# Optimization experiments

Measured on AMD Instinct MI355X. Metric: run time of the kernel, lower is better.

The kernel has to match this reference:

```python
import jax, jax.numpy as jnp
import numpy as np

LN_EPS = 1e-5

def setup_inputs() -> dict:
    key = jax.random.key(0)
    B, S, D = 4, 2048, 1024
    ks = jax.random.split(key, 8)
    sc = 1.0 / np.sqrt(D)
    inp = {
        'x': jax.random.normal(ks[0], (B, S, D), jnp.float32),
        'Wq': jax.random.normal(ks[1], (D, D), jnp.float32) * sc,
        'bq': jnp.zeros((D,), jnp.float32),
        'Wk': jax.random.normal(ks[2], (D, D), jnp.float32) * sc,
        'bk': jnp.zeros((D,), jnp.float32),
        'Wv': jax.random.normal(ks[3], (D, D), jnp.float32) * sc,
        'bv': jnp.zeros((D,), jnp.float32),
        'Wo': jax.random.normal(ks[4], (D, D), jnp.float32) * sc,
        'bo': jnp.zeros((D,), jnp.float32),
        'Wg_val': jax.random.normal(ks[5], (D, D), jnp.float32) * sc,
        'bg_val': jnp.zeros((D,), jnp.float32),
        'Wg_gate': jax.random.normal(ks[6], (D, D), jnp.float32) * sc,
        'bg_gate': jnp.zeros((D,), jnp.float32),
        'gamma': jnp.ones((D,), jnp.float32),
        'beta': jnp.zeros((D,), jnp.float32),
    }
    return inp


def reference(x, Wq, bq, Wk, bk, Wv, bv, Wo, bo, Wg_val, bg_val, Wg_gate, bg_gate, gamma, beta):
    # x: [B,S,D]
    q = jnp.einsum('bsd,de->bse', x, Wq) + bq
    k = jnp.einsum('bsd,de->bse', x, Wk) + bk
    v = jnp.einsum('bsd,de->bse', x, Wv) + bv
    scale = 1.0 / jnp.sqrt(jnp.asarray(q.shape[-1], q.dtype))
    qk = jnp.einsum('bqe,bke->bqk', q, k) * scale  # [B,S,S]
    a = jax.nn.softmax(qk, axis=-1)
    out = jnp.einsum('bqk,bke->bqe', a, v)
    out = jnp.einsum('bse,ed->bsd', out, Wo) + bo
    # GLU residual on q, then LayerNorm
    glu = (jnp.einsum('bse,ed->bsd', q, Wg_val) + bg_val) * jax.nn.sigmoid(jnp.einsum('bse,ed->bsd', q, Wg_gate) + bg_gate)
    out = out + glu
    mu = jnp.mean(out, axis=-1, keepdims=True)
    var = jnp.var(out, axis=-1, keepdims=True)
    out = (out - mu) * jax.lax.rsqrt(var + LN_EPS) * gamma + beta
    return out
```

## Files before the change

### kernel.cpp

```cpp
#include <hip/hip_runtime.h>
#include <hip/hip_bf16.h>
#include <cstdint>


typedef __bf16 bf16x8 __attribute__((ext_vector_type(8)));
typedef __bf16 bf16x4 __attribute__((ext_vector_type(4)));
typedef float f32x4 __attribute__((ext_vector_type(4)));

#define SYNC() do { asm volatile("" ::: "memory"); __builtin_amdgcn_s_barrier(); asm volatile("" ::: "memory"); } while (0)
#define WAITV(n) asm volatile("s_waitcnt vmcnt(" #n ")" ::: "memory")

__device__ __forceinline__ void gload16(const void* g, void* l) {
    __builtin_amdgcn_global_load_lds(
        (__attribute__((address_space(1))) void*)(uintptr_t)g,
        (__attribute__((address_space(3))) void*)(uintptr_t)l,
        16, 0, 0);
}

#define STAGE(buf, isB, half, kt)                                                        \
    do {                                                                                 \
        const __hip_bfloat16* g_ = (isB) ? gB : gA;                                      \
        const int ld_ = (isB) ? ldb : lda;                                               \
        char* l_ = smem + (buf) * 65536 + (isB) * 32768 + (half) * 16384;                \
        gload16(g_ + (long)((half) * 128 + r0) * ld_ + (kt) * 64 + s0 * 8, l_ + tid * 16);        \
        gload16(g_ + (long)((half) * 128 + r1) * ld_ + (kt) * 64 + s1 * 8, l_ + 8192 + tid * 16); \
    } while (0)
#define LDA_(dst, buf, mh, mi, kk)                                                       \
    do {                                                                                 \
        const int lr_ = wm * 64 + (mi) * 16 + fr;                                        \
        const int sl_ = ((kk) * 4 + kg) ^ (lr_ & 7);                                     \
        dst = *(const bf16x8*)(smem + (buf) * 65536 + (mh) * 16384 + lr_ * 128 + sl_ * 16); \
    } while (0)
#define LDB_(dst, buf, nh, ni, kk)                                                       \
    do {                                                                                 \
        const int lr_ = wn * 32 + (ni) * 16 + fr;                                        \
        const int sl_ = ((kk) * 4 + kg) ^ (lr_ & 7);                                     \
        dst = *(const bf16x8*)(smem + (buf) * 65536 + 32768 + (nh) * 16384 + lr_ * 128 + sl_ * 16); \
    } while (0)
#define MFMA_QUAD2(mh, nh, AV, BV)                                                       \
    do {                                                                                 \
        __builtin_amdgcn_s_setprio(1);                                                   \
        _Pragma("unroll")                                                                \
        for (int mi = 0; mi < 4; ++mi)                                                   \
            _Pragma("unroll")                                                            \
            for (int ni = 0; ni < 2; ++ni)                                               \
                _Pragma("unroll")                                                        \
                for (int kk = 0; kk < 2; ++kk)                                           \
                    acc[mh][nh][mi][ni] = __builtin_amdgcn_mfma_f32_16x16x32_bf16(       \
                        AV[mi][kk], BV[ni][kk], acc[mh][nh][mi][ni], 0, 0, 0);           \
        __builtin_amdgcn_s_setprio(0);                                                   \
    } while (0)

#define GEMM256_BODY(NT)                                                                 \
    STAGE(0, 0, 0, 0);                                                                   \
    STAGE(0, 1, 0, 0);                                                                   \
    STAGE(0, 1, 1, 0);                                                                   \
    STAGE(0, 0, 1, 0);                                                                   \
    WAITV(4);                                                                            \
    SYNC();                                                                              \
    _Pragma("unroll")                                                                    \
    for (int mi = 0; mi < 4; ++mi) { LDA_(av0[mi][0], 0, 0, mi, 0); LDA_(av0[mi][1], 0, 0, mi, 1); } \
    _Pragma("unroll")                                                                    \
    for (int ni = 0; ni < 2; ++ni) { LDB_(bv0[ni][0], 0, 0, ni, 0); LDB_(bv0[ni][1], 0, 0, ni, 1); } \
    for (int t = 0; t < (NT) - 1; ++t) {                                                 \
        const int c = t & 1;                                                             \
        STAGE(c ^ 1, 0, 0, t + 1);                                                       \
        MFMA_QUAD2(0, 0, av0, bv0);                                                      \
        _Pragma("unroll")                                                                \
        for (int ni = 0; ni < 2; ++ni) { LDB_(bv1[ni][0], c, 1, ni, 0); LDB_(bv1[ni][1], c, 1, ni, 1); } \
        WAITV(4);                                                                        \
        SYNC();                                                                          \
        STAGE(c ^ 1, 1, 0, t + 1);                                                       \
        MFMA_QUAD2(0, 1, av0, bv1);                                                      \
        _Pragma("unroll")                                                                \
        for (int mi = 0; mi < 4; ++mi) { LDA_(av1[mi][0], c, 1, mi, 0); LDA_(av1[mi][1], c, 1, mi, 1); } \
        WAITV(4);                                                                        \
        SYNC();                                                                          \
        STAGE(c ^ 1, 1, 1, t + 1);                                                       \
        MFMA_QUAD2(1, 1, av1, bv1);                                                      \
        SYNC();                                                                          \
        STAGE(c ^ 1, 0, 1, t + 1);                                                       \
        MFMA_QUAD2(1, 0, av1, bv0);                                                      \
        WAITV(4);                                                                        \
        SYNC();                                                                          \
        _Pragma("unroll")                                                                \
        for (int mi = 0; mi < 4; ++mi) { LDA_(av0[mi][0], c ^ 1, 0, mi, 0); LDA_(av0[mi][1], c ^ 1, 0, mi, 1); } \
        _Pragma("unroll")                                                                \
        for (int ni = 0; ni < 2; ++ni) { LDB_(bv0[ni][0], c ^ 1, 0, ni, 0); LDB_(bv0[ni][1], c ^ 1, 0, ni, 1); } \
    }                                                                                    \
    {            \
        const int c = ((NT) - 1) & 1;                                                    \
        MFMA_QUAD2(0, 0, av0, bv0);                                                      \
        WAITV(2);                                                                        \
        SYNC();                                                                          \
        _Pragma("unroll")                                                                \
        for (int ni = 0; ni < 2; ++ni) { LDB_(bv1[ni][0], c, 1, ni, 0); LDB_(bv1[ni][1], c, 1, ni, 1); } \
        MFMA_QUAD2(0, 1, av0, bv1);                                                      \
        WAITV(0);                                                                        \
        SYNC();                                                                          \
        _Pragma("unroll")                                                                \
        for (int mi = 0; mi < 4; ++mi) { LDA_(av1[mi][0], c, 1, mi, 0); LDA_(av1[mi][1], c, 1, mi, 1); } \
        MFMA_QUAD2(1, 1, av1, bv1);                                                      \
        MFMA_QUAD2(1, 0, av1, bv0);                                                      \
    }

template <int EPI>
__global__ __launch_bounds__(512, 1) void gemm256(
    const __hip_bfloat16* __restrict__ A1, int lda1,
    const __hip_bfloat16* __restrict__ A2, int lda2, int nsplit,
    const __hip_bfloat16* __restrict__ Bt,
    __hip_bfloat16* __restrict__ Cout, const float* __restrict__ bias, float scale,
    int K, int ldb, int ldc,
    long strideA, long strideB, long strideC)
{
    __shared__ __align__(16) char smem[131072];

    const int b = blockIdx.z;
    const int tid = threadIdx.x;
    const int lane = tid & 63;
    const int wm = (tid >> 6) & 1;
    const int wn = (tid >> 6) >> 1;

    const bool sel2 = ((int)blockIdx.y * 256) >= nsplit;
    const __hip_bfloat16* A = sel2 ? A2 : A1;
    const int lda = sel2 ? lda2 : lda1;

    const __hip_bfloat16* gA = A + (long)b * strideA + (long)blockIdx.x * 256 * lda;
    const __hip_bfloat16* gB = Bt + (long)b * strideB + (long)blockIdx.y * 256 * ldb;

    const int r0 = tid >> 3;
    const int s0 = (tid & 7) ^ (r0 & 7);
    const int r1 = r0 + 64;
    const int s1 = (tid & 7) ^ (r1 & 7);
    const int fr = lane & 15;
    const int kg = lane >> 4;

    f32x4 acc[2][2][4][2];
#pragma unroll
    for (int mh = 0; mh < 2; ++mh)
#pragma unroll
        for (int nh = 0; nh < 2; ++nh)
#pragma unroll
            for (int mi = 0; mi < 4; ++mi)
#pragma unroll
                for (int ni = 0; ni < 2; ++ni) acc[mh][nh][mi][ni] = {0.f, 0.f, 0.f, 0.f};
    bf16x8 av0[4][2], av1[4][2], bv0[2][2], bv1[2][2];

    const int NT = K >> 6;
    GEMM256_BODY(NT)

    const long row0 = (long)blockIdx.x * 256 + wm * 64 + (lane >> 4) * 4;
    const long col0 = (long)blockIdx.y * 256 + wn * 32 + (lane & 15);
#pragma unroll
    for (int mh = 0; mh < 2; ++mh) {
#pragma unroll
        for (int nh = 0; nh < 2; ++nh) {
#pragma unroll
            for (int ni = 0; ni < 2; ++ni) {
                const long col = col0 + nh * 128 + ni * 16;
                const float bval = (EPI == 0 && bias != nullptr) ? bias[col] : 0.f;
#pragma unroll
                for (int mi = 0; mi < 4; ++mi) {
                    const long row = row0 + mh * 128 + mi * 16;
#pragma unroll
                    for (int i = 0; i < 4; ++i) {
                        const float v = (EPI == 1) ? acc[mh][nh][mi][ni][i] * scale
                                                   : acc[mh][nh][mi][ni][i] + bval;
                        Cout[(long)b * strideC + (row + i) * (long)ldc + col] = __float2bfloat16(v);
                    }
                }
            }
        }
    }
}

__global__ __launch_bounds__(512, 1) void gemm256_dual(
    const __hip_bfloat16* __restrict__ wvT, const __hip_bfloat16* __restrict__ xb,
    const __hip_bfloat16* __restrict__ Qp, const __hip_bfloat16* __restrict__ wggT,
    __hip_bfloat16* __restrict__ vt, __hip_bfloat16* __restrict__ T1G,
    const float* __restrict__ bvp, const float* __restrict__ bgg)
{
    __shared__ __align__(16) char smem[131072];

    const int bid = blockIdx.x;
    const bool isVt = bid < 128;
    const int tid = threadIdx.x;
    const int lane = tid & 63;
    const int wm = (tid >> 6) & 1;
    const int wn = (tid >> 6) >> 1;

    int mx, my, lda, ldb;
    const __hip_bfloat16 *Aop, *Bop;
    if (isVt) { mx = bid >> 5; my = bid & 31; Aop = wvT; lda = 1024; Bop = xb;   ldb = 1024; }
    else { const int t2 = bid - 128; mx = t2 >> 2; my = t2 & 3; Aop = Qp; lda = 2048; Bop = wggT; ldb = 1024; }

    const __hip_bfloat16* gA = Aop + (long)mx * 256 * lda;
    const __hip_bfloat16* gB = Bop + (long)my * 256 * ldb;

    const int r0 = tid >> 3;
    const int s0 = (tid & 7) ^ (r0 & 7);
    const int r1 = r0 + 64;
    const int s1 = (tid & 7) ^ (r1 & 7);
    const int fr = lane & 15;
    const int kg = lane >> 4;

    f32x4 acc[2][2][4][2];
#pragma unroll
    for (int mh = 0; mh < 2; ++mh)
#pragma unroll
        for (int nh = 0; nh < 2; ++nh)
#pragma unroll
            for (int mi = 0; mi < 4; ++mi)
#pragma unroll
                for (int ni = 0; ni < 2; ++ni) acc[mh][nh][mi][ni] = {0.f, 0.f, 0.f, 0.f};
    bf16x8 av0[4][2], av1[4][2], bv0[2][2], bv1[2][2];

    GEMM256_BODY(16)

    const long row0 = (long)mx * 256 + wm * 64 + (lane >> 4) * 4;
    const long col0 = (long)my * 256 + wn * 32 + (lane & 15);
    if (isVt) {
#pragma unroll
        for (int mh = 0; mh < 2; ++mh)
#pragma unroll
            for (int nh = 0; nh < 2; ++nh)
#pragma unroll
                for (int ni = 0; ni < 2; ++ni) {
                    const long col = col0 + nh * 128 + ni * 16;
                    const long vb = col >> 11, vs = col & 2047;
#pragma unroll
                    for (int mi = 0; mi < 4; ++mi) {
#pragma unroll
                        for (int i = 0; i < 4; ++i) {
                            const long row = row0 + mh * 128 + mi * 16 + i;
                            vt[(vb << 21) + row * 2048 + vs] =
                                __float2bfloat16(acc[mh][nh][mi][ni][i] + bvp[row]);
                        }
                    }
                }
    } else {
#pragma unroll
        for (int mh = 0; mh < 2; ++mh)
#pragma unroll
            for (int nh = 0; nh < 2; ++nh)
#pragma unroll
                for (int ni = 0; ni < 2; ++ni) {
                    const long col = col0 + nh * 128 + ni * 16;
                    const float bval = bgg[col];
#pragma unroll
                    for (int mi = 0; mi < 4; ++mi) {
                        const long row = row0 + mh * 128 + mi * 16;
#pragma unroll
                        for (int i = 0; i < 4; ++i)
                            T1G[(row + i) * 3072 + 2048 + col] =
                                __float2bfloat16(acc[mh][nh][mi][ni][i] + bval);
                    }
                }
    }
}

__global__ __launch_bounds__(512, 1) void gemm_tn128(
    const __hip_bfloat16* __restrict__ A, int lda,
    const __hip_bfloat16* __restrict__ Bt,
    __hip_bfloat16* __restrict__ Cout, const float* __restrict__ bias,
    int K, int ldb, int ldc,
    long strideA, long strideB, long strideC)
{
    __shared__ __align__(16) char smem[147456];

    const int b = blockIdx.z;
    const int tid = threadIdx.x;
    const int lane = tid & 63;
    const int wid = tid >> 6;
    const int wm = wid & 3;
    const int wn = wid >> 2;

    const __hip_bfloat16* gA = A + (long)b * strideA + (long)blockIdx.x * 256 * lda;
    const __hip_bfloat16* gB = Bt + (long)b * strideB + (long)blockIdx.y * 128 * ldb;

    const int r0 = tid >> 3, r1 = r0 + 64;
    const int s0 = (tid & 7) ^ (r0 & 7);
    const int s1 = (tid & 7) ^ (r1 & 7);

#define STG_A(base_, h_, kt_)                                                                              \
    do {                                                                                                   \
        gload16(gA + (long)((h_) * 128 + r0) * lda + (kt_) * 64 + s0 * 8, (base_) + (h_) * 16384 + tid * 16);        \
        gload16(gA + (long)((h_) * 128 + r1) * lda + (kt_) * 64 + s1 * 8, (base_) + (h_) * 16384 + 8192 + tid * 16); \
    } while (0)
#define STG_B(base_, kt_)                                                                                  \
    do {                                                                                                   \
        gload16(gB + (long)r0 * ldb + (kt_) * 64 + s0 * 8, (base_) + 32768 + tid * 16);                    \
        gload16(gB + (long)r1 * ldb + (kt_) * 64 + s1 * 8, (base_) + 32768 + 8192 + tid * 16);             \
    } while (0)

    const int fr = lane & 15;
    const int kg = lane >> 4;

#define LD_A(dst, base_, mi_, kk_)                                                        \
    do {                                                                                  \
        const int row_ = wm * 64 + (mi_) * 16 + fr;                                       \
        const int sl_ = ((kk_) * 4 + kg) ^ (row_ & 7);                                    \
        dst = *(const bf16x8*)((base_) + row_ * 128 + sl_ * 16);                          \
    } while (0)
#define LD_B(dst, base_, ni_, kk_)                                                        \
    do {                                                                                  \
        const int row_ = wn * 64 + (ni_) * 16 + fr;                                       \
        const int sl_ = ((kk_) * 4 + kg) ^ (row_ & 7);                                    \
        dst = *(const bf16x8*)((base_) + 32768 + row_ * 128 + sl_ * 16);                  \
    } while (0)

    f32x4 acc[4][4];
#pragma unroll
    for (int mi = 0; mi < 4; ++mi)
#pragma unroll
        for (int ni = 0; ni < 4; ++ni) acc[mi][ni] = {0.f, 0.f, 0.f, 0.f};

    const int NT = K >> 6;

    STG_A(smem, 0, 0); STG_A(smem, 1, 0); STG_B(smem, 0);
    STG_A(smem + 49152, 0, 1); STG_A(smem + 49152, 1, 1); STG_B(smem + 49152, 1);
    WAITV(6);
    SYNC();

    int bi = 0;
    for (int t = 0; t < NT; ++t) {
        char* base = smem + bi * 49152;
        if (t + 2 < NT) {
            int bs = bi + 2; if (bs >= 3) bs -= 3;
            char* sb = smem + bs * 49152;
            STG_A(sb, 0, t + 2); STG_A(sb, 1, t + 2); STG_B(sb, t + 2);
        }
        bf16x8 av[4], bvv[4];
#pragma unroll
        for (int kk = 0; kk < 2; ++kk) {
#pragma unroll
            for (int mi = 0; mi < 4; ++mi) LD_A(av[mi], base, mi, kk);
#pragma unroll
            for (int ni = 0; ni < 4; ++ni) LD_B(bvv[ni], base, ni, kk);
            __builtin_amdgcn_s_setprio(1);
#pragma unroll
            for (int mi = 0; mi < 4; ++mi)
#pragma unroll
                for (int ni = 0; ni < 4; ++ni)
                    acc[mi][ni] = __builtin_amdgcn_mfma_f32_16x16x32_bf16(av[mi], bvv[ni], acc[mi][ni], 0, 0, 0);
            __builtin_amdgcn_s_setprio(0);
        }
        if (t + 2 < NT) { WAITV(6); SYNC(); }
        else if (t + 1 < NT) { WAITV(0); SYNC(); }
        bi = (bi + 1 == 3) ? 0 : bi + 1;
    }

    const long row0 = (long)blockIdx.x * 256 + wm * 64 + (lane >> 4) * 4;
    const long col0 = (long)blockIdx.y * 128 + wn * 64 + (lane & 15);
#pragma unroll
    for (int ni = 0; ni < 4; ++ni) {
        const long col = col0 + ni * 16;
        const float bval = (bias != nullptr) ? bias[col] : 0.f;
#pragma unroll
        for (int mi = 0; mi < 4; ++mi) {
            const long row = row0 + mi * 16;
#pragma unroll
            for (int i = 0; i < 4; ++i)
                Cout[(long)b * strideC + (row + i) * (long)ldc + col] = __float2bfloat16(acc[mi][ni][i] + bval);
        }
    }
#undef STG_A
#undef STG_B
#undef LD_A
#undef LD_B
}

__global__ __launch_bounds__(256) void transpose6(
    const float* __restrict__ W0, const float* __restrict__ W1, const float* __restrict__ W2,
    const float* __restrict__ W3, const float* __restrict__ W4, const float* __restrict__ W5,
    __hip_bfloat16* __restrict__ dst)
{
    __shared__ float tile[32][33];
    const int z = blockIdx.z;
    const float* pin = (z == 0) ? W0 : (z == 1) ? W1 : (z == 2) ? W2 : (z == 3) ? W3 : (z == 4) ? W4 : W5;
    __hip_bfloat16* pout = dst + (long)z * 1024 * 1024;
    const int tx = threadIdx.x, ty = threadIdx.y;
    const int c0 = blockIdx.x * 32, r0 = blockIdx.y * 32;
#pragma unroll
    for (int j = 0; j < 4; ++j)
        tile[ty + j * 8][tx] = pin[(long)(r0 + ty + j * 8) * 1024 + c0 + tx];
    __syncthreads();
#pragma unroll
    for (int j = 0; j < 4; ++j)
        pout[(long)(c0 + ty + j * 8) * 1024 + r0 + tx] = __float2bfloat16(tile[tx][ty + j * 8]);
}

__global__ __launch_bounds__(256) void f32_to_bf16_vec(
    const float* __restrict__ in, __hip_bfloat16* __restrict__ out, long n4)
{
    const long i = (long)blockIdx.x * 256 + threadIdx.x;
    if (i >= n4) return;
    const float4 v = ((const float4*)in)[i];
    union { __hip_bfloat16 h[4]; ushort4 u; } cv;
    cv.h[0] = __float2bfloat16(v.x);
    cv.h[1] = __float2bfloat16(v.y);
    cv.h[2] = __float2bfloat16(v.z);
    cv.h[3] = __float2bfloat16(v.w);
    ((ushort4*)out)[i] = cv.u;
}

__global__ __launch_bounds__(256) void concat_bias(
    const float* __restrict__ bq, const float* __restrict__ bk, const float* __restrict__ bv,
    const float* __restrict__ bo, const float* __restrict__ bgv, const float* __restrict__ bgg,
    float* __restrict__ out)
{
    const int i = blockIdx.x * 256 + threadIdx.x;
    float v;
    if (i < 1024) v = bq[i];
    else if (i < 2048) v = bk[i - 1024];
    else if (i < 3072) v = bv[i - 2048];
    else if (i < 4096) v = bo[i - 3072];
    else if (i < 5120) v = bgv[i - 4096];
    else v = bgg[i - 5120];
    out[i] = v;
}

__global__ __launch_bounds__(256) void softmax_kernel(
    const __hip_bfloat16* __restrict__ S, __hip_bfloat16* __restrict__ P)
{
    const long row = blockIdx.x;
    const __hip_bfloat16* s = S + row * 2048;
    __hip_bfloat16* p = P + row * 2048;
    const int t = threadIdx.x;
    const bf16x8 v8 = *(const bf16x8*)(s + t * 8);
    float v[8];
    float mx = -1e30f;
#pragma unroll
    for (int j = 0; j < 8; ++j) { v[j] = (float)v8[j]; mx = fmaxf(mx, v[j]); }
#pragma unroll
    for (int off = 32; off; off >>= 1) mx = fmaxf(mx, __shfl_xor(mx, off));
    __shared__ float wred[4];
    __shared__ float wsum[4];
    const int w = t >> 6;
    if ((t & 63) == 0) wred[w] = mx;
    __syncthreads();
    mx = fmaxf(fmaxf(wred[0], wred[1]), fmaxf(wred[2], wred[3]));
    float sum = 0.f;
#pragma unroll
    for (int j = 0; j < 8; ++j) { v[j] = __expf(v[j] - mx); sum += v[j]; }
#pragma unroll
    for (int off = 32; off; off >>= 1) sum += __shfl_xor(sum, off);
    if ((t & 63) == 0) wsum[w] = sum;
    __syncthreads();
    sum = wsum[0] + wsum[1] + wsum[2] + wsum[3];
    const float inv = 1.0f / sum;
    bf16x8 o8;
#pragma unroll
    for (int j = 0; j < 8; ++j) o8[j] = (__bf16)(v[j] * inv);
    *(bf16x8*)(p + t * 8) = o8;
}

__global__ __launch_bounds__(256) void glu_ln_kernel(
    const __hip_bfloat16* __restrict__ T1G,
    const float* __restrict__ gamma, const float* __restrict__ beta, float* __restrict__ out)
{
    const long row = blockIdx.x;
    const __hip_bfloat16* pr = T1G + row * 3072;
    const int t = threadIdx.x;
    const int c0 = t * 4;
    const bf16x4 t1 = *(const bf16x4*)(pr + c0);
    const bf16x4 gv = *(const bf16x4*)(pr + 1024 + c0);
    const bf16x4 gg = *(const bf16x4*)(pr + 2048 + c0);
    float y[4];
    float s = 0.f, ss = 0.f;
#pragma unroll
    for (int j = 0; j < 4; ++j) {
        const float g = (float)gv[j] * (1.0f / (1.0f + __expf(-(float)gg[j])));
        const float val = (float)t1[j] + g;
        y[j] = val; s += val; ss += val * val;
    }
#pragma unroll
    for (int off = 32; off; off >>= 1) { s += __shfl_xor(s, off); ss += __shfl_xor(ss, off); }
    __shared__ float rs[4], rss[4];
    const int w = t >> 6;
    if ((t & 63) == 0) { rs[w] = s; rss[w] = ss; }
    __syncthreads();
    s = rs[0] + rs[1] + rs[2] + rs[3];
    ss = rss[0] + rss[1] + rss[2] + rss[3];
    const float mu = s * (1.0f / 1024.0f);
    const float var = ss * (1.0f / 1024.0f) - mu * mu;
    const float r = rsqrtf(var + 1e-5f);
    const float4 gm = *(const float4*)(gamma + c0);
    const float4 bt = *(const float4*)(beta + c0);
    float4 o;
    o.x = (y[0] - mu) * r * gm.x + bt.x;
    o.y = (y[1] - mu) * r * gm.y + bt.y;
    o.z = (y[2] - mu) * r * gm.z + bt.z;
    o.w = (y[3] - mu) * r * gm.w + bt.w;
    *(float4*)(out + row * 1024 + c0) = o;
}

extern "C" void kernel_launch(void* const* d_in, const int* in_sizes, int n_in,
                              void* d_out, int out_size, void* d_ws, size_t ws_size,
                              hipStream_t stream)
{
    const int B = 4, S = 2048, D = 1024;
    const float* x    = (const float*)d_in[0];
    const float* Wq   = (const float*)d_in[1];
    const float* bq   = (const float*)d_in[2];
    const float* Wk   = (const float*)d_in[3];
    const float* bk   = (const float*)d_in[4];
    const float* Wv   = (const float*)d_in[5];
    const float* bv   = (const float*)d_in[6];
    const float* Wo   = (const float*)d_in[7];
    const float* bo   = (const float*)d_in[8];
    const float* Wgv  = (const float*)d_in[9];
    const float* bgv  = (const float*)d_in[10];
    const float* Wgg  = (const float*)d_in[11];
    const float* bgg  = (const float*)d_in[12];
    const float* gamma = (const float*)d_in[13];
    const float* beta  = (const float*)d_in[14];
    float* out = (float*)d_out;

    char* ws = (char*)d_ws;
    size_t off = 0;
    auto take = [&](size_t bytes) { char* p = ws + off; off += (bytes + 255) & ~(size_t)255; return p; };

    __hip_bfloat16* wcat   = (__hip_bfloat16*)take((size_t)6 * D * D * 2);
    float*          bcat   = (float*)take((size_t)6 * D * 4);
    __hip_bfloat16* xb     = (__hip_bfloat16*)take((size_t)B * S * D * 2);
    __hip_bfloat16* QKb    = (__hip_bfloat16*)take((size_t)B * S * 2 * D * 2);
    __hip_bfloat16* Vtb    = (__hip_bfloat16*)take((size_t)B * S * D * 2);
    __hip_bfloat16* scoresb = (__hip_bfloat16*)take((size_t)B * S * S * 2);
    __hip_bfloat16* Pb     = (__hip_bfloat16*)take((size_t)B * S * S * 2);
    __hip_bfloat16* Oatt   = (__hip_bfloat16*)take((size_t)B * S * D * 2);
    __hip_bfloat16* T1G    = (__hip_bfloat16*)take((size_t)B * S * 3 * D * 2);

    const long SD = (long)S * D, SS = (long)S * S, S2D = (long)S * 2 * D;
    const float att_scale = 0.03125f;
    const __hip_bfloat16* Qb = QKb;
    const __hip_bfloat16* Kb = QKb + D;

    f32_to_bf16_vec<<<dim3((unsigned)((long)B * S * D / 4 / 256)), dim3(256), 0, stream>>>(x, xb, (long)B * S * D / 4);
    transpose6<<<dim3(D / 32, D / 32, 6), dim3(32, 8), 0, stream>>>(Wq, Wk, Wv, Wo, Wgv, Wgg, wcat);
    concat_bias<<<dim3(24), dim3(256), 0, stream>>>(bq, bk, bv, bo, bgv, bgg, bcat);

    gemm256<0><<<dim3(B * S / 256, 2 * D / 256, 1), dim3(512), 0, stream>>>(
        xb, D, xb, D, 1 << 30, wcat, QKb, bcat, 1.f,
        D, D, 2 * D, 0, 0, 0);

    gemm256_dual<<<dim3(256), dim3(512), 0, stream>>>(
        wcat + (size_t)2 * D * D, xb, QKb, wcat + (size_t)5 * D * D,
        Vtb, T1G, bcat + 2 * D, bcat + 5 * D);

    gemm256<1><<<dim3(S / 256, S / 256, B), dim3(512), 0, stream>>>(
        Qb, 2 * D, Qb, 2 * D, 1 << 30, Kb, scoresb, nullptr, att_scale,
        D, 2 * D, S, S2D, S2D, SS);

    softmax_kernel<<<dim3(B * S), dim3(256), 0, stream>>>(scoresb, Pb);

    gemm_tn128<<<dim3(S / 256, D / 128, B), dim3(512), 0, stream>>>(
        Pb, S, Vtb, Oatt, nullptr, S, S, D, SS, SD, SD);

    gemm256<0><<<dim3(B * S / 256, 2 * D / 256, 1), dim3(512), 0, stream>>>(
        Oatt, D, QKb, 2 * D, D, wcat + (size_t)3 * D * D, T1G, bcat + 3 * D, 1.f,
        D, D, 3 * D, 0, 0, 0);

    glu_ln_kernel<<<dim3(B * S), dim3(256), 0, stream>>>(T1G, gamma, beta, out);
}
```

Before: 228.4 us.

## Restructure GEMM main loop into deeper quarter-tile prefetch pipeline

Measured after the change: 235.4 us. 1.03x slower.

```diff
diff --git a/kernel.cpp b/kernel.cpp
--- a/kernel.cpp
+++ b/kernel.cpp
@@ -9,6 +9,7 @@
 
 #define SYNC() do { asm volatile("" ::: "memory"); __builtin_amdgcn_s_barrier(); asm volatile("" ::: "memory"); } while (0)
 #define WAITV(n) asm volatile("s_waitcnt vmcnt(" #n ")" ::: "memory")
+#define LGKM0() do { asm volatile("s_waitcnt lgkmcnt(0)" ::: "memory"); __builtin_amdgcn_sched_barrier(0); } while (0)
 
 __device__ __forceinline__ void gload16(const void* g, void* l) {
     __builtin_amdgcn_global_load_lds(
@@ -37,7 +38,7 @@
         const int sl_ = ((kk) * 4 + kg) ^ (lr_ & 7);                                     \
         dst = *(const bf16x8*)(smem + (buf) * 65536 + 32768 + (nh) * 16384 + lr_ * 128 + sl_ * 16); \
     } while (0)
-#define MFMA_QUAD2(mh, nh, AV, BV)                                                       \
+#define MFMA_Q(mh, nh, AV, BV)                                                           \
     do {                                                                                 \
         __builtin_amdgcn_s_setprio(1);                                                   \
         _Pragma("unroll")                                                                \
@@ -52,56 +53,44 @@
     } while (0)
 
 #define GEMM256_BODY(NT)                                                                 \
-    STAGE(0, 0, 0, 0);                                                                   \
-    STAGE(0, 1, 0, 0);                                                                   \
-    STAGE(0, 1, 1, 0);                                                                   \
-    STAGE(0, 0, 1, 0);                                                                   \
-    WAITV(4);                                                                            \
+    STAGE(0, 0, 0, 0); STAGE(0, 1, 0, 0); STAGE(0, 1, 1, 0); STAGE(0, 0, 1, 0);          \
+    STAGE(1, 0, 0, 1); STAGE(1, 1, 0, 1); STAGE(1, 1, 1, 1);                             \
+    WAITV(6);                                                                            \
     SYNC();                                                                              \
-    _Pragma("unroll")                                                                    \
-    for (int mi = 0; mi < 4; ++mi) { LDA_(av0[mi][0], 0, 0, mi, 0); LDA_(av0[mi][1], 0, 0, mi, 1); } \
-    _Pragma("unroll")                                                                    \
-    for (int ni = 0; ni < 2; ++ni) { LDB_(bv0[ni][0], 0, 0, ni, 0); LDB_(bv0[ni][1], 0, 0, ni, 1); } \
-    for (int t = 0; t < (NT) - 1; ++t) {                                                 \
-        const int c = t & 1;                                                             \
-        STAGE(c ^ 1, 0, 0, t + 1);                                                       \
-        MFMA_QUAD2(0, 0, av0, bv0);                                                      \
+    for (int j = 0; j < (NT); ++j) {                                                     \
+        const int bu = j & 1;                                                            \
+        const int ob = bu ^ 1;                                                           \
+        const bool dA1 = (j + 1) < (NT);                                                 \
+        const bool d2  = (j + 2) < (NT);                                                 \
+                                          \
         _Pragma("unroll")                                                                \
-        for (int ni = 0; ni < 2; ++ni) { LDB_(bv1[ni][0], c, 1, ni, 0); LDB_(bv1[ni][1], c, 1, ni, 1); } \
-        WAITV(4);                                                                        \
+        for (int mi = 0; mi < 4; ++mi) { LDA_(av[mi][0], bu, 0, mi, 0); LDA_(av[mi][1], bu, 0, mi, 1); } \
+        _Pragma("unroll")                                                                \
+        for (int ni = 0; ni < 2; ++ni) { LDB_(bvA[ni][0], bu, 0, ni, 0); LDB_(bvA[ni][1], bu, 0, ni, 1); } \
+        if (dA1) STAGE(ob, 0, 1, j + 1);                                                 \
+        SYNC(); LGKM0();                                                                 \
+        MFMA_Q(0, 0, av, bvA);                                                           \
         SYNC();                                                                          \
-        STAGE(c ^ 1, 1, 0, t + 1);                                                       \
-        MFMA_QUAD2(0, 1, av0, bv1);                                                      \
+              \
         _Pragma("unroll")                                                                \
-        for (int mi = 0; mi < 4; ++mi) { LDA_(av1[mi][0], c, 1, mi, 0); LDA_(av1[mi][1], c, 1, mi, 1); } \
-        WAITV(4);                                                                        \
+        for (int ni = 0; ni < 2; ++ni) { LDB_(bvB[ni][0], bu, 1, ni, 0); LDB_(bvB[ni][1], bu, 1, ni, 1); } \
+        if (d2) STAGE(bu, 0, 0, j + 2);                                                  \
+        SYNC(); LGKM0();                                                                 \
+        MFMA_Q(0, 1, av, bvB);                                                           \
         SYNC();                                                                          \
-        STAGE(c ^ 1, 1, 1, t + 1);                                                       \
-        MFMA_QUAD2(1, 1, av1, bv1);                                                      \
+                          \
+        _Pragma("unroll")                                                                \
+        for (int mi = 0; mi < 4; ++mi) { LDA_(av[mi][0], bu, 1, mi, 0); LDA_(av[mi][1], bu, 1, mi, 1); } \
+        if (d2) STAGE(bu, 1, 0, j + 2);                                                  \
+        SYNC(); LGKM0();                                                                 \
+        MFMA_Q(1, 1, av, bvB);                                                           \
         SYNC();                                                                          \
-        STAGE(c ^ 1, 0, 1, t + 1);                                                       \
-        MFMA_QUAD2(1, 0, av1, bv0);                                                      \
-        WAITV(4);                                                                        \
+                 \
+        if (d2) STAGE(bu, 1, 1, j + 2);                                                  \
+        if (d2) { WAITV(6); }                                                            \
+        else if (dA1) { WAITV(0); }                                                      \
         SYNC();                                                                          \
-        _Pragma("unroll")                                                                \
-        for (int mi = 0; mi < 4; ++mi) { LDA_(av0[mi][0], c ^ 1, 0, mi, 0); LDA_(av0[mi][1], c ^ 1, 0, mi, 1); } \
-        _Pragma("unroll")                                                                \
-        for (int ni = 0; ni < 2; ++ni) { LDB_(bv0[ni][0], c ^ 1, 0, ni, 0); LDB_(bv0[ni][1], c ^ 1, 0, ni, 1); } \
-    }                                                                                    \
-    {            \
-        const int c = ((NT) - 1) & 1;                                                    \
-        MFMA_QUAD2(0, 0, av0, bv0);                                                      \
-        WAITV(2);                                                                        \
-        SYNC();                                                                          \
-        _Pragma("unroll")                                                                \
-        for (int ni = 0; ni < 2; ++ni) { LDB_(bv1[ni][0], c, 1, ni, 0); LDB_(bv1[ni][1], c, 1, ni, 1); } \
-        MFMA_QUAD2(0, 1, av0, bv1);                                                      \
-        WAITV(0);                                                                        \
-        SYNC();                                                                          \
-        _Pragma("unroll")                                                                \
-        for (int mi = 0; mi < 4; ++mi) { LDA_(av1[mi][0], c, 1, mi, 0); LDA_(av1[mi][1], c, 1, mi, 1); } \
-        MFMA_QUAD2(1, 1, av1, bv1);                                                      \
-        MFMA_QUAD2(1, 0, av1, bv0);                                                      \
+        MFMA_Q(1, 0, av, bvA);                                                           \
     }
 
 template <int EPI>
@@ -144,7 +133,7 @@
             for (int mi = 0; mi < 4; ++mi)
 #pragma unroll
                 for (int ni = 0; ni < 2; ++ni) acc[mh][nh][mi][ni] = {0.f, 0.f, 0.f, 0.f};
-    bf16x8 av0[4][2], av1[4][2], bv0[2][2], bv1[2][2];
+    bf16x8 av[4][2], bvA[2][2], bvB[2][2];
 
     const int NT = K >> 6;
     GEMM256_BODY(NT)
@@ -213,7 +202,7 @@
             for (int mi = 0; mi < 4; ++mi)
 #pragma unroll
                 for (int ni = 0; ni < 2; ++ni) acc[mh][nh][mi][ni] = {0.f, 0.f, 0.f, 0.f};
-    bf16x8 av0[4][2], av1[4][2], bv0[2][2], bv1[2][2];
+    bf16x8 av[4][2], bvA[2][2], bvB[2][2];
 
     GEMM256_BODY(16)
 
```
